# Kernel tuning notes

Hardware: AMD Instinct MI355X
Metric: run time of the kernel (lower is better)

## Reference

```python
import jax, jax.numpy as jnp
import numpy as np

WS = 8    # window size
DM = 64   # d_model
DI = 128  # d_inner = 2*d_model (expand=2)
DS = 16   # d_state
DR = 4    # dt_rank = ceil(d_model/16)
K = 4     # scan directions


def setup_inputs() -> dict:
    key = jax.random.key(0)
    ks = jax.random.split(key, 8)
    B, H, W = 2, 128, 128
    x = jax.random.normal(ks[0], (B, DM, H, W), jnp.float32)
    in_proj_w = jax.random.normal(ks[1], (2 * DI, DM), jnp.float32) * 0.02
    conv_w = jax.random.normal(ks[2], (DI, 1, 3, 3), jnp.float32) * 0.1
    conv_b = jnp.zeros((DI,), jnp.float32)
    x_proj_w = jax.random.normal(ks[3], (K, DR + 2 * DS, DI), jnp.float32) * 0.02
    dt_projs_w = jax.random.normal(ks[4], (K, DI, DR), jnp.float32) * 0.1
    dt_projs_b = jax.random.uniform(ks[5], (K, DI), jnp.float32, -6.0, -3.0)
    A_logs = jnp.log(jnp.tile(jnp.arange(1, DS + 1, dtype=jnp.float32), (K, DI, 1)))
    Ds = jnp.ones((K, DI), jnp.float32)
    ln_g = jnp.ones((DI,), jnp.float32)
    ln_b = jnp.zeros((DI,), jnp.float32)
    out_proj_w = jax.random.normal(ks[6], (DM, DI), jnp.float32) * 0.02
    return dict(x=x, in_proj_w=in_proj_w, conv_w=conv_w, conv_b=conv_b,
                x_proj_w=x_proj_w, dt_projs_w=dt_projs_w, dt_projs_b=dt_projs_b,
                A_logs=A_logs, Ds=Ds, ln_g=ln_g, ln_b=ln_b, out_proj_w=out_proj_w)


def _ss2d(x, in_proj_w, conv_w, conv_b, x_proj_w, dt_projs_w, dt_projs_b,
          A_logs, Ds, ln_g, ln_b, out_proj_w):
    # x: (Bw, DM, h, w) -- one 8x8 window per batch element
    Bw, _, h, w = x.shape
    L = h * w
    xhwc = x.transpose(0, 2, 3, 1)                      # (Bw,h,w,DM)
    xz = xhwc @ in_proj_w.T                             # (Bw,h,w,2*DI)
    xc, z = jnp.split(xz, 2, axis=-1)
    xc = xc.transpose(0, 3, 1, 2)                       # (Bw,DI,h,w)
    xc = jax.lax.conv_general_dilated(
        xc, conv_w, (1, 1), 'SAME', feature_group_count=DI,
        dimension_numbers=('NCHW', 'OIHW', 'NCHW')) + conv_b[None, :, None, None]
    xc = jax.nn.silu(xc)
    # 4-direction cross-scan: hw, wh, reversed hw, reversed wh
    x_hw = xc.reshape(Bw, DI, L)
    x_wh = xc.transpose(0, 1, 3, 2).reshape(Bw, DI, L)
    xs = jnp.stack([x_hw, x_wh, x_hw[..., ::-1], x_wh[..., ::-1]], axis=1)  # (Bw,K,DI,L)
    x_dbl = jnp.einsum('bkdl,kcd->bkcl', xs, x_proj_w)
    dt_lo, Bmat, Cmat = jnp.split(x_dbl, [DR, DR + DS], axis=2)
    dt = jnp.einsum('bkrl,kdr->bkdl', dt_lo, dt_projs_w)
    dt = jax.nn.softplus(dt + dt_projs_b[None, :, :, None])  # (Bw,K,DI,L)
    A = -jnp.exp(A_logs)                                     # (K,DI,DS)

    def step(hst, inp):
        u_t, dt_t, B_t, C_t = inp  # (Bw,K,DI),(Bw,K,DI),(Bw,K,DS),(Bw,K,DS)
        dA = jnp.exp(dt_t[..., None] * A)                       # (Bw,K,DI,DS)
        hst = hst * dA + (dt_t * u_t)[..., None] * B_t[:, :, None, :]
        y = jnp.einsum('bkds,bks->bkd', hst, C_t)
        return hst, y

    seq = (jnp.moveaxis(xs, -1, 0), jnp.moveaxis(dt, -1, 0),
           jnp.moveaxis(Bmat, -1, 0), jnp.moveaxis(Cmat, -1, 0))
    h0 = jnp.zeros((Bw, K, DI, DS), xs.dtype)
    _, ys = jax.lax.scan(step, h0, seq)                  # (L,Bw,K,DI)
    ys = jnp.moveaxis(ys, 0, -1) + Ds[None, :, :, None] * xs  # (Bw,K,DI,L)
    # merge directions (undo flips / wh transpose)
    y = (ys[:, 0]
         + ys[:, 2][..., ::-1]
         + ys[:, 1].reshape(Bw, DI, w, h).transpose(0, 1, 3, 2).reshape(Bw, DI, L)
         + ys[:, 3][..., ::-1].reshape(Bw, DI, w, h).transpose(0, 1, 3, 2).reshape(Bw, DI, L))
    y = y.reshape(Bw, DI, h, w).transpose(0, 2, 3, 1)    # (Bw,h,w,DI)
    mu = y.mean(-1, keepdims=True)
    var = y.var(-1, keepdims=True)
    y = (y - mu) * jax.lax.rsqrt(var + 1e-5) * ln_g + ln_b
    y = y * jax.nn.silu(z)
    out = y @ out_proj_w.T                               # (Bw,h,w,DM)
    return out.transpose(0, 3, 1, 2)


def reference(x, in_proj_w, conv_w, conv_b, x_proj_w, dt_projs_w, dt_projs_b,
              A_logs, Ds, ln_g, ln_b, out_proj_w):
    B, D, H, W = x.shape
    nh, nw = H // WS, W // WS
    # window partition: b d (nh hs) (nw ws) -> (b nh nw) d hs ws
    xw = x.reshape(B, D, nh, WS, nw, WS).transpose(0, 2, 4, 1, 3, 5)
    xw = xw.reshape(B * nh * nw, D, WS, WS)
    yw = _ss2d(xw, in_proj_w, conv_w, conv_b, x_proj_w, dt_projs_w, dt_projs_b,
               A_logs, Ds, ln_g, ln_b, out_proj_w)
    # window merge
    y = yw.reshape(B, nh, nw, D, WS, WS).transpose(0, 3, 1, 4, 2, 5)
    return y.reshape(B, D, H, W)
```

## Files before the change

kernel.cpp:

```cpp
#include <hip/hip_runtime.h>

#define L_HW (128*128)

__device__ __forceinline__ int transp(int p){ return ((p&7)<<3)|(p>>3); }

#define K1_XIN  0
#define K1_WBUF 4352
#define K1_XCP  8448
#define K1_XOUT 0
#define K1_SMEM 12608

__global__ __launch_bounds__(512, 4)
void k1_gemm(const float* __restrict__ x,
             const float* __restrict__ in_proj_w,
             const float* __restrict__ conv_w,
             const float* __restrict__ conv_b,
             float* __restrict__ xct_g,
             float* __restrict__ z_g)
{
    __shared__ float sm[K1_SMEM];
    const int t = threadIdx.x;
    const int win = blockIdx.x >> 2, q = blockIdx.x & 3;
    const int b = win >> 8, ih = (win >> 4) & 15, iw = win & 15;
    const float* xwin = x + ((size_t)b*64)*L_HW + ih*8*128 + iw*8;

    {
        const int ch = t >> 3, r = t & 7;
        const float* src = xwin + (size_t)ch*L_HW + r*128;
        float4 v0 = *(const float4*)(src);
        float4 v1 = *(const float4*)(src + 4);
        float* dst = sm + K1_XIN + ch;
        const int p0 = r*8;
        dst[(p0+0)*68]=v0.x; dst[(p0+1)*68]=v0.y; dst[(p0+2)*68]=v0.z; dst[(p0+3)*68]=v0.w;
        dst[(p0+4)*68]=v1.x; dst[(p0+5)*68]=v1.y; dst[(p0+6)*68]=v1.z; dst[(p0+7)*68]=v1.w;
    }
    {
        const float* wsrc = in_proj_w + q*4096;
        *(float4*)(sm + K1_WBUF + t*4)        = *(const float4*)(wsrc + t*4);
        *(float4*)(sm + K1_WBUF + (t+512)*4)  = *(const float4*)(wsrc + (t+512)*4);
    }
    __syncthreads();

    const int p = t & 63, og = t >> 6;
    float a0=0,a1=0,a2=0,a3=0,a4=0,a5=0,a6=0,a7=0;
    {
        const float* wrow = sm + K1_WBUF + og*8*64;
#define K1ACC(J, A) { float4 wv = *(const float4*)(wrow + (J)*64 + chq*4); \
        A = fmaf(xv.x,wv.x, fmaf(xv.y,wv.y, fmaf(xv.z,wv.z, fmaf(xv.w,wv.w, A)))); }
        #pragma unroll
        for (int chq = 0; chq < 16; ++chq) {
            float4 xv = *(const float4*)(sm + K1_XIN + p*68 + chq*4);
            K1ACC(0,a0) K1ACC(1,a1) K1ACC(2,a2) K1ACC(3,a3)
            K1ACC(4,a4) K1ACC(5,a5) K1ACC(6,a6) K1ACC(7,a7)
        }
#undef K1ACC
    }

    if (q >= 2) {
        float* zw = z_g + (size_t)win*8192 + ((q-2)*64)*64 + p;
        zw[(og*8+0)*64]=a0; zw[(og*8+1)*64]=a1; zw[(og*8+2)*64]=a2; zw[(og*8+3)*64]=a3;
        zw[(og*8+4)*64]=a4; zw[(og*8+5)*64]=a5; zw[(og*8+6)*64]=a6; zw[(og*8+7)*64]=a7;
        return;
    }

    {
        float* xp = sm + K1_XCP + og*8*65 + p;
        xp[0]=a0; xp[65]=a1; xp[130]=a2; xp[195]=a3;
        xp[260]=a4; xp[325]=a5; xp[390]=a6; xp[455]=a7;
    }
    __syncthreads();

    {
        const int dloc = t & 63, qq = t >> 6;
        const int dg = q*64 + dloc;
        const float* cwp = conv_w + dg*9;
        const float c0=cwp[0],c1=cwp[1],c2=cwp[2],c3=cwp[3],c4=cwp[4],
                    c5=cwp[5],c6=cwp[6],c7=cwp[7],c8=cwp[8];
        const float cb = conv_b[dg];
        const float* xc = sm + K1_XCP + dloc*65;
        #pragma unroll
        for (int jj = 0; jj < 8; ++jj) {
            const int px = qq*8 + jj;
            const int r = px >> 3, c = px & 7;
            float a = cb;
            if (r > 0) {
                if (c > 0) a = fmaf(xc[px-9], c0, a);
                a = fmaf(xc[px-8], c1, a);
                if (c < 7) a = fmaf(xc[px-7], c2, a);
            }
            if (c > 0) a = fmaf(xc[px-1], c3, a);
            a = fmaf(xc[px], c4, a);
            if (c < 7) a = fmaf(xc[px+1], c5, a);
            if (r < 7) {
                if (c > 0) a = fmaf(xc[px+7], c6, a);
                a = fmaf(xc[px+8], c7, a);
                if (c < 7) a = fmaf(xc[px+9], c8, a);
            }
            sm[K1_XOUT + px*68 + dloc] = a / (1.f + __expf(-a));
        }
    }
    __syncthreads();

    {
        float* dst = xct_g + (size_t)win*8192 + q*64;
        #pragma unroll
        for (int i = 0; i < 2; ++i) {
            const int idx4 = i*512 + t;
            const int pp = idx4 >> 4, dg = idx4 & 15;
            float4 v = *(const float4*)(sm + K1_XOUT + pp*68 + dg*4);
            *(float4*)(dst + pp*128 + dg*4) = v;
        }
    }
}

#define K2_WL 4096
#define K2_XD 6400
#define K2_SMEM 8768

__global__ __launch_bounds__(256, 4)
void k2_xproj(const float* __restrict__ xct_g,
              const float* __restrict__ x_proj_w,
              float* __restrict__ xdbl_g)
{
    __shared__ float sm[K2_SMEM];
    const int t = threadIdx.x;
    const int win = blockIdx.x >> 2, k = blockIdx.x & 3;
    const int p = t & 63, jg = t >> 6;
    float a0=0,a1=0,a2=0,a3=0,a4=0,a5=0,a6=0,a7=0,a8=0;

    for (int h = 0; h < 2; ++h) {
        __syncthreads();
        #pragma unroll
        for (int i = 0; i < 4; ++i) {
            const int idx4 = i*256 + t;
            const int pp = idx4 >> 4, dg = idx4 & 15;
            float4 v = *(const float4*)(xct_g + (size_t)win*8192 + pp*128 + h*64 + dg*4);
            *(float4*)(sm + pp*64 + ((dg ^ (pp&7))<<2)) = v;
        }
        #pragma unroll
        for (int i = 0; i < 3; ++i) {
            const int idx4 = i*256 + t;
            if (idx4 < 576) {
                const int r = idx4 >> 4, dg = idx4 & 15;
                float4 v = *(const float4*)(x_proj_w + (size_t)(k*36 + r)*128 + h*64 + dg*4);
                *(float4*)(sm + K2_WL + r*64 + dg*4) = v;
            }
        }
        __syncthreads();
        const float* wb = sm + K2_WL + jg*9*64;
#define K2ACC(J, A) { float4 wv = *(const float4*)(wb + (J)*64 + dg*4); \
        A = fmaf(xv.x,wv.x, fmaf(xv.y,wv.y, fmaf(xv.z,wv.z, fmaf(xv.w,wv.w, A)))); }
        #pragma unroll
        for (int dg = 0; dg < 16; ++dg) {
            float4 xv = *(const float4*)(sm + p*64 + ((dg ^ (p&7))<<2));
            K2ACC(0,a0) K2ACC(1,a1) K2ACC(2,a2) K2ACC(3,a3) K2ACC(4,a4)
            K2ACC(5,a5) K2ACC(6,a6) K2ACC(7,a7) K2ACC(8,a8)
        }
#undef K2ACC
    }
    __syncthreads();

    {
        const int l = (k==0) ? p : (k==1) ? transp(p) : (k==2) ? (63-p) : (63 - transp(p));
        float* dp = sm + K2_XD + l*37 + jg*9;
        dp[0]=a0; dp[1]=a1; dp[2]=a2; dp[3]=a3; dp[4]=a4;
        dp[5]=a5; dp[6]=a6; dp[7]=a7; dp[8]=a8;
    }
    __syncthreads();

    {
        float* dst = xdbl_g + ((size_t)win*4 + k)*2304;
        #pragma unroll
        for (int i = 0; i < 9; ++i) {
            const int idx = i*256 + t;
            const int l2 = idx / 36, c = idx - l2*36;
            dst[idx] = sm[K2_XD + l2*37 + c];
        }
    }
}

#define F_XD 0
#define F_YM 0
#define F_U  9216
#define F_MU 17408
#define F_RS 17472
#define F_SMEM 17536

#define HSTEP(I, E, BC, CC) { h##I = fmaf(h##I, (E), dtu*(BC)); y = fmaf(h##I, (CC), y); }

__global__ __launch_bounds__(512, 4)
void k3_all(const float* __restrict__ xct_g,
            const float* __restrict__ z_g,
            const float* __restrict__ xdbl_g,
            const float* __restrict__ dt_projs_w,
            const float* __restrict__ dt_projs_b,
            const float* __restrict__ A_logs,
            const float* __restrict__ Ds,
            const float* __restrict__ ln_g,
            const float* __restrict__ ln_b,
            const float* __restrict__ out_proj_w,
            float* __restrict__ y_g,
            float* __restrict__ out)
{
    __shared__ float sm[F_SMEM];
    const int t = threadIdx.x;
    const int win = blockIdx.x;

    #pragma unroll
    for (int i = 0; i < 5; ++i) {
        const int idx4 = i*512 + t;
        if (idx4 < 2304) {
            float4 v = *(const float4*)(xdbl_g + (size_t)win*9216 + idx4*4);
            *(float4*)(sm + F_XD + idx4*4) = v;
        }
    }
    #pragma unroll
    for (int i = 0; i < 4; ++i) {
        const int idx4 = i*512 + t;
        float4 v = *(const float4*)(xct_g + (size_t)win*8192 + idx4*4);
        *(float4*)(sm + F_U + idx4*4) = v;
    }
    __syncthreads();

    {
        const int k = t >> 7, d = t & 127;
        const int kd = t;
        const float* alp = A_logs + kd*16;
        const float A0 = -__expf(alp[0]);
        bool fast = true;
        #pragma unroll
        for (int s = 1; s < 16; ++s) {
            float a = -__expf(alp[s]);
            fast = fast && (fabsf(a - (float)(s+1)*A0) <= 1e-4f * fabsf(a));
        }
        const float4 wv = *(const float4*)(dt_projs_w + kd*4);
        const float dtb = dt_projs_b[kd];
        float h0=0,h1=0,h2=0,h3=0,h4=0,h5=0,h6=0,h7=0,
              h8=0,h9=0,h10=0,h11=0,h12=0,h13=0,h14=0,h15=0;
        const float* XDk = sm + F_XD + k*2304;
        const float* ul = sm + F_U + d;
        float* yw = y_g + ((size_t)win*4 + k)*8192 + d;

        if (fast) {
            for (int l = 0; l < 64; ++l) {
                const float* row = XDk + l*36;
                float4 d4 = *(const float4*)(row);
                float4 b0 = *(const float4*)(row+4),  b1 = *(const float4*)(row+8);
                float4 b2 = *(const float4*)(row+12), b3 = *(const float4*)(row+16);
                float4 c0 = *(const float4*)(row+20), c1 = *(const float4*)(row+24);
                float4 c2 = *(const float4*)(row+28), c3 = *(const float4*)(row+32);
                float dtraw = dtb + wv.x*d4.x + wv.y*d4.y + wv.z*d4.z + wv.w*d4.w;
                float dt = (dtraw > 20.f) ? dtraw : __logf(1.f + __expf(dtraw));
                const int lr = 63 - l;
                const int p = (k==0)?l : (k==1)?transp(l) : (k==2)?lr : transp(lr);
                const float u = ul[p*128];
                const float dtu = dt * u;
                const float r  = __expf(dt * A0);
                const float r2 = r*r, r4 = r2*r2, r8 = r4*r4;
                const float e3 = r2*r, e5 = r4*r, e6 = r4*r2, e7 = r4*e3;
                const float e9 = r8*r, e10 = r8*r2, e11 = r8*e3, e12 = r8*r4;
                const float e13 = r8*e5, e14 = r8*e6, e15 = r8*e7, e16 = r8*r8;
                float y = 0.f;
                HSTEP(0,  r,   b0.x, c0.x)  HSTEP(1,  r2,  b0.y, c0.y)
                HSTEP(2,  e3,  b0.z, c0.z)  HSTEP(3,  r4,  b0.w, c0.w)
                HSTEP(4,  e5,  b1.x, c1.x)  HSTEP(5,  e6,  b1.y, c1.y)
                HSTEP(6,  e7,  b1.z, c1.z)  HSTEP(7,  r8,  b1.w, c1.w)
                HSTEP(8,  e9,  b2.x, c2.x)  HSTEP(9,  e10, b2.y, c2.y)
                HSTEP(10, e11, b2.z, c2.z)  HSTEP(11, e12, b2.w, c2.w)
                HSTEP(12, e13, b3.x, c3.x)  HSTEP(13, e14, b3.y, c3.y)
                HSTEP(14, e15, b3.z, c3.z)  HSTEP(15, e16, b3.w, c3.w)
                yw[l*128] = y;
            }
        } else {
            const float A1=-__expf(alp[1]), A2=-__expf(alp[2]), A3=-__expf(alp[3]),
                        A4=-__expf(alp[4]), A5=-__expf(alp[5]), A6=-__expf(alp[6]),
                        A7=-__expf(alp[7]), A8=-__expf(alp[8]), A9=-__expf(alp[9]),
                        A10=-__expf(alp[10]), A11=-__expf(alp[11]), A12=-__expf(alp[12]),
                        A13=-__expf(alp[13]), A14=-__expf(alp[14]), A15=-__expf(alp[15]);
            for (int l = 0; l < 64; ++l) {
                const float* row = XDk + l*36;
                float4 d4 = *(const float4*)(row);
                float4 b0 = *(const float4*)(row+4),  b1 = *(const float4*)(row+8);
                float4 b2 = *(const float4*)(row+12), b3 = *(const float4*)(row+16);
                float4 c0 = *(const float4*)(row+20), c1 = *(const float4*)(row+24);
                float4 c2 = *(const float4*)(row+28), c3 = *(const float4*)(row+32);
                float dtraw = dtb + wv.x*d4.x + wv.y*d4.y + wv.z*d4.z + wv.w*d4.w;
                float dt = (dtraw > 20.f) ? dtraw : __logf(1.f + __expf(dtraw));
                const int lr = 63 - l;
                const int p = (k==0)?l : (k==1)?transp(l) : (k==2)?lr : transp(lr);
                const float u = ul[p*128];
                const float dtu = dt * u;
                float y = 0.f;
                HSTEP(0,  __expf(dt*A0),  b0.x, c0.x)  HSTEP(1,  __expf(dt*A1),  b0.y, c0.y)
                HSTEP(2,  __expf(dt*A2),  b0.z, c0.z)  HSTEP(3,  __expf(dt*A3),  b0.w, c0.w)
                HSTEP(4,  __expf(dt*A4),  b1.x, c1.x)  HSTEP(5,  __expf(dt*A5),  b1.y, c1.y)
                HSTEP(6,  __expf(dt*A6),  b1.z, c1.z)  HSTEP(7,  __expf(dt*A7),  b1.w, c1.w)
                HSTEP(8,  __expf(dt*A8),  b2.x, c2.x)  HSTEP(9,  __expf(dt*A9),  b2.y, c2.y)
                HSTEP(10, __expf(dt*A10), b2.z, c2.z)  HSTEP(11, __expf(dt*A11), b2.w, c2.w)
                HSTEP(12, __expf(dt*A12), b3.x, c3.x)  HSTEP(13, __expf(dt*A13), b3.y, c3.y)
                HSTEP(14, __expf(dt*A14), b3.z, c3.z)  HSTEP(15, __expf(dt*A15), b3.w, c3.w)
                yw[l*128] = y;
            }
        }
    }
    __syncthreads();

    {
        const int d2 = t & 127, pq = t >> 7;
        const float Dsum = Ds[d2] + Ds[128+d2] + Ds[256+d2] + Ds[384+d2];
        const float* yg0 = y_g + ((size_t)win*4 + 0)*8192 + d2;
        const float* yg1 = y_g + ((size_t)win*4 + 1)*8192 + d2;
        const float* yg2 = y_g + ((size_t)win*4 + 2)*8192 + d2;
        const float* yg3 = y_g + ((size_t)win*4 + 3)*8192 + d2;
        const float* uc  = sm + F_U + d2;
        #pragma unroll
        for (int i = 0; i < 16; ++i) {
            const int p = pq*16 + i;
            const int tp = transp(p);
            float v = yg0[p*128] + yg1[tp*128] + yg2[(63-p)*128] + yg3[(63-tp)*128]
                    + Dsum * uc[p*128];
            sm[F_YM + d2*65 + p] = v;
        }
    }
    __syncthreads();

    {
        const int px = t >> 3, j = t & 7;
        float s1 = 0.f, s2 = 0.f;
        #pragma unroll
        for (int i = 0; i < 16; ++i) {
            float v = sm[F_YM + (j*16 + i)*65 + px];
            s1 += v; s2 += v*v;
        }
        s1 += __shfl_xor(s1,1); s2 += __shfl_xor(s2,1);
        s1 += __shfl_xor(s1,2); s2 += __shfl_xor(s2,2);
        s1 += __shfl_xor(s1,4); s2 += __shfl_xor(s2,4);
        if (j == 0) {
            float mu  = s1 * 0.0078125f;
            float var = s2 * 0.0078125f - mu*mu;
            sm[F_MU + px] = mu;
            sm[F_RS + px] = rsqrtf(var + 1e-5f);
        }
    }
    __syncthreads();

    {
        const int p = t & 63, dblk = (t >> 6) * 16;
        const float mu = sm[F_MU + p], rs = sm[F_RS + p];
        const float* zb = z_g + (size_t)win*8192 + p;
        #pragma unroll
        for (int i = 0; i < 16; ++i) {
            const int d = dblk + i;
            float yv = sm[F_YM + d*65 + p];
            float yh = (yv - mu)*rs*ln_g[d] + ln_b[d];
            float zv = zb[d*64];
            sm[F_YM + d*65 + p] = yh * (zv / (1.f + __expf(-zv)));
        }
    }
    __syncthreads();

    {
        const int p = t & 63, m0 = (t >> 6) * 8;
        float o0=0,o1=0,o2=0,o3=0,o4=0,o5=0,o6=0,o7=0;
#define OACC(J, O) { float4 wq = *(const float4*)(out_proj_w + (m0+(J))*128 + dq*4); \
        O = fmaf(y0,wq.x, fmaf(y1,wq.y, fmaf(y2,wq.z, fmaf(y3,wq.w, O)))); }
        #pragma unroll
        for (int dq = 0; dq < 32; ++dq) {
            float y0 = sm[F_YM + (dq*4+0)*65 + p];
            float y1 = sm[F_YM + (dq*4+1)*65 + p];
            float y2 = sm[F_YM + (dq*4+2)*65 + p];
            float y3 = sm[F_YM + (dq*4+3)*65 + p];
            OACC(0,o0) OACC(1,o1) OACC(2,o2) OACC(3,o3)
            OACC(4,o4) OACC(5,o5) OACC(6,o6) OACC(7,o7)
        }
#undef OACC
        const int b = win >> 8, ih = (win>>4)&15, iw = win&15;
        float* op = out + ((size_t)b*64)*L_HW + (ih*8 + (p>>3))*128 + iw*8 + (p&7);
        op[(size_t)(m0+0)*L_HW]=o0; op[(size_t)(m0+1)*L_HW]=o1;
        op[(size_t)(m0+2)*L_HW]=o2; op[(size_t)(m0+3)*L_HW]=o3;
        op[(size_t)(m0+4)*L_HW]=o4; op[(size_t)(m0+5)*L_HW]=o5;
        op[(size_t)(m0+6)*L_HW]=o6; op[(size_t)(m0+7)*L_HW]=o7;
    }
}
#undef HSTEP

extern "C" void kernel_launch(void* const* d_in, const int* in_sizes, int n_in,
                              void* d_out, int out_size, void* d_ws, size_t ws_size,
                              hipStream_t stream) {
    const float* x          = (const float*)d_in[0];
    const float* in_proj_w  = (const float*)d_in[1];
    const float* conv_w     = (const float*)d_in[2];
    const float* conv_b     = (const float*)d_in[3];
    const float* x_proj_w   = (const float*)d_in[4];
    const float* dt_projs_w = (const float*)d_in[5];
    const float* dt_projs_b = (const float*)d_in[6];
    const float* A_logs     = (const float*)d_in[7];
    const float* Ds         = (const float*)d_in[8];
    const float* ln_g       = (const float*)d_in[9];
    const float* ln_b       = (const float*)d_in[10];
    const float* out_proj_w = (const float*)d_in[11];
    float* out = (float*)d_out;

    float* xct  = (float*)d_ws;
    float* zb   = xct + 4194304;
    float* xdbl = zb  + 4194304;
    float* yg   = xdbl + 1179648;

    k1_gemm<<<dim3(2048), dim3(512), 0, stream>>>(x, in_proj_w, conv_w, conv_b, xct, zb);
    k2_xproj<<<dim3(2048), dim3(256), 0, stream>>>(xct, x_proj_w, xdbl);
    k3_all<<<dim3(512), dim3(512), 0, stream>>>(
        xct, zb, xdbl, dt_projs_w, dt_projs_b, A_logs, Ds, ln_g, ln_b,
        out_proj_w, yg, out);
}
```

Measured before the change: 157.3 us.

## Merge scan directions in shared memory instead of round-tripping through global

The selective scan no longer writes per-direction outputs to a global y buffer and reads them back. Each thread writes its step output to a small shared staging area every 4 steps, and 128 threads then accumulate the four directions into the merged shared tile. The u input is read straight from global instead of being staged in shared memory, and the per-step y sum is split into four accumulators to shorten the dependency chain. The cost is two block barriers per 4-step chunk (32 in total) and a serial merge by a quarter of the threads.

```diff
diff --git a/kernel.cpp b/kernel.cpp
--- a/kernel.cpp
+++ b/kernel.cpp
@@ -180,13 +180,13 @@
 }
 
 #define F_XD 0
-#define F_YM 0
-#define F_U  9216
-#define F_MU 17408
-#define F_RS 17472
-#define F_SMEM 17536
-
-#define HSTEP(I, E, BC, CC) { h##I = fmaf(h##I, (E), dtu*(BC)); y = fmaf(h##I, (CC), y); }
+#define F_YC 9216
+#define F_YM 11264
+#define F_MU 19584
+#define F_RS 19648
+#define F_SMEM 19712
+
+#define HSTEP(I, E, BC, CC, Y) { h##I = fmaf(h##I, (E), dtu*(BC)); Y = fmaf(h##I, (CC), Y); }
 
 __global__ __launch_bounds__(512, 4)
 void k3_all(const float* __restrict__ xct_g,
@@ -199,7 +199,6 @@
             const float* __restrict__ ln_g,
             const float* __restrict__ ln_b,
             const float* __restrict__ out_proj_w,
-            float* __restrict__ y_g,
             float* __restrict__ out)
 {
     __shared__ float sm[F_SMEM];
@@ -214,38 +213,53 @@
             *(float4*)(sm + F_XD + idx4*4) = v;
         }
     }
+    for (int i = t; i < 8320; i += 512) sm[F_YM + i] = 0.f;
+
+    const int k = t >> 7, d = t & 127;
+    const int kd = t;
+    const float* alp = A_logs + kd*16;
+    const float A0 = -__expf(alp[0]);
+    bool fastp = true;
     #pragma unroll
-    for (int i = 0; i < 4; ++i) {
-        const int idx4 = i*512 + t;
-        float4 v = *(const float4*)(xct_g + (size_t)win*8192 + idx4*4);
-        *(float4*)(sm + F_U + idx4*4) = v;
-    }
-    __syncthreads();
-
-    {
-        const int k = t >> 7, d = t & 127;
-        const int kd = t;
-        const float* alp = A_logs + kd*16;
-        const float A0 = -__expf(alp[0]);
-        bool fast = true;
-        #pragma unroll
-        for (int s = 1; s < 16; ++s) {
-            float a = -__expf(alp[s]);
-            fast = fast && (fabsf(a - (float)(s+1)*A0) <= 1e-4f * fabsf(a));
-        }
-        const float4 wv = *(const float4*)(dt_projs_w + kd*4);
-        const float dtb = dt_projs_b[kd];
-        float h0=0,h1=0,h2=0,h3=0,h4=0,h5=0,h6=0,h7=0,
-              h8=0,h9=0,h10=0,h11=0,h12=0,h13=0,h14=0,h15=0;
-        const float* XDk = sm + F_XD + k*2304;
-        const float* ul = sm + F_U + d;
-        float* yw = y_g + ((size_t)win*4 + k)*8192 + d;
-
-        if (fast) {
-            for (int l = 0; l < 64; ++l) {
+    for (int s = 1; s < 16; ++s) {
+        float a = -__expf(alp[s]);
+        fastp = fastp && (fabsf(a - (float)(s+1)*A0) <= 1e-4f * fabsf(a));
+    }
+    const int allfast = __syncthreads_and(fastp ? 1 : 0);
+
+    const float4 wv = *(const float4*)(dt_projs_w + kd*4);
+    const float dtb = dt_projs_b[kd];
+    float h0=0,h1=0,h2=0,h3=0,h4=0,h5=0,h6=0,h7=0,
+          h8=0,h9=0,h10=0,h11=0,h12=0,h13=0,h14=0,h15=0;
+    const float* XDk = sm + F_XD + k*2304;
+    const float* ub = xct_g + (size_t)win*8192 + d;
+
+#define MERGE_CHUNK(C) { \
+        __syncthreads(); \
+        if (t < 128) { \
+            const int dd = t; \
+            float* ymr = sm + F_YM + dd*65; \
+            _Pragma("unroll") \
+            for (int j = 0; j < 4; ++j) { \
+                const int l = (C)*4 + j; \
+                const int lr = 63 - l; \
+                const float* ycb = sm + F_YC + j*512 + dd; \
+                ymr[l]          += ycb[0]; \
+                ymr[transp(l)]  += ycb[128]; \
+                ymr[lr]         += ycb[256]; \
+                ymr[transp(lr)] += ycb[384]; \
+            } \
+        } \
+        __syncthreads(); }
+
+    if (allfast) {
+        for (int c = 0; c < 16; ++c) {
+            #pragma unroll
+            for (int j = 0; j < 4; ++j) {
+                const int l = c*4 + j;
                 const float* row = XDk + l*36;
                 float4 d4 = *(const float4*)(row);
-                float4 b0 = *(const float4*)(row+4),  b1 = *(const float4*)(row+8);
+                float4 b0 = *(const float4*)(row+4),  float4_b1 = *(const float4*)(row+8);
                 float4 b2 = *(const float4*)(row+12), b3 = *(const float4*)(row+16);
                 float4 c0 = *(const float4*)(row+20), c1 = *(const float4*)(row+24);
                 float4 c2 = *(const float4*)(row+28), c3 = *(const float4*)(row+32);
@@ -253,34 +267,39 @@
                 float dt = (dtraw > 20.f) ? dtraw : __logf(1.f + __expf(dtraw));
                 const int lr = 63 - l;
                 const int p = (k==0)?l : (k==1)?transp(l) : (k==2)?lr : transp(lr);
-                const float u = ul[p*128];
+                const float u = ub[p*128];
                 const float dtu = dt * u;
                 const float r  = __expf(dt * A0);
                 const float r2 = r*r, r4 = r2*r2, r8 = r4*r4;
                 const float e3 = r2*r, e5 = r4*r, e6 = r4*r2, e7 = r4*e3;
                 const float e9 = r8*r, e10 = r8*r2, e11 = r8*e3, e12 = r8*r4;
                 const float e13 = r8*e5, e14 = r8*e6, e15 = r8*e7, e16 = r8*r8;
-                float y = 0.f;
-                HSTEP(0,  r,   b0.x, c0.x)  HSTEP(1,  r2,  b0.y, c0.y)
-                HSTEP(2,  e3,  b0.z, c0.z)  HSTEP(3,  r4,  b0.w, c0.w)
-                HSTEP(4,  e5,  b1.x, c1.x)  HSTEP(5,  e6,  b1.y, c1.y)
-                HSTEP(6,  e7,  b1.z, c1.z)  HSTEP(7,  r8,  b1.w, c1.w)
-                HSTEP(8,  e9,  b2.x, c2.x)  HSTEP(9,  e10, b2.y, c2.y)
-                HSTEP(10, e11, b2.z, c2.z)  HSTEP(11, e12, b2.w, c2.w)
-                HSTEP(12, e13, b3.x, c3.x)  HSTEP(13, e14, b3.y, c3.y)
-                HSTEP(14, e15, b3.z, c3.z)  HSTEP(15, e16, b3.w, c3.w)
-                yw[l*128] = y;
+                float ay0 = 0.f, ay1 = 0.f, ay2 = 0.f, ay3 = 0.f;
+                HSTEP(0,  r,   b0.x, c0.x, ay0)  HSTEP(1,  r2,  b0.y, c0.y, ay1)
+                HSTEP(2,  e3,  b0.z, c0.z, ay2)  HSTEP(3,  r4,  b0.w, c0.w, ay3)
+                HSTEP(4,  e5,  float4_b1.x, c1.x, ay0)  HSTEP(5,  e6,  float4_b1.y, c1.y, ay1)
+                HSTEP(6,  e7,  float4_b1.z, c1.z, ay2)  HSTEP(7,  r8,  float4_b1.w, c1.w, ay3)
+                HSTEP(8,  e9,  b2.x, c2.x, ay0)  HSTEP(9,  e10, b2.y, c2.y, ay1)
+                HSTEP(10, e11, b2.z, c2.z, ay2)  HSTEP(11, e12, b2.w, c2.w, ay3)
+                HSTEP(12, e13, b3.x, c3.x, ay0)  HSTEP(13, e14, b3.y, c3.y, ay1)
+                HSTEP(14, e15, b3.z, c3.z, ay2)  HSTEP(15, e16, b3.w, c3.w, ay3)
+                sm[F_YC + j*512 + t] = (ay0 + ay1) + (ay2 + ay3);
             }
-        } else {
-            const float A1=-__expf(alp[1]), A2=-__expf(alp[2]), A3=-__expf(alp[3]),
-                        A4=-__expf(alp[4]), A5=-__expf(alp[5]), A6=-__expf(alp[6]),
-                        A7=-__expf(alp[7]), A8=-__expf(alp[8]), A9=-__expf(alp[9]),
-                        A10=-__expf(alp[10]), A11=-__expf(alp[11]), A12=-__expf(alp[12]),
-                        A13=-__expf(alp[13]), A14=-__expf(alp[14]), A15=-__expf(alp[15]);
-            for (int l = 0; l < 64; ++l) {
+            MERGE_CHUNK(c)
+        }
+    } else {
+        const float A1=-__expf(alp[1]), A2=-__expf(alp[2]), A3=-__expf(alp[3]),
+                    A4=-__expf(alp[4]), A5=-__expf(alp[5]), A6=-__expf(alp[6]),
+                    A7=-__expf(alp[7]), A8=-__expf(alp[8]), A9=-__expf(alp[9]),
+                    A10=-__expf(alp[10]), A11=-__expf(alp[11]), A12=-__expf(alp[12]),
+                    A13=-__expf(alp[13]), A14=-__expf(alp[14]), A15=-__expf(alp[15]);
+        for (int c = 0; c < 16; ++c) {
+            #pragma unroll
+            for (int j = 0; j < 4; ++j) {
+                const int l = c*4 + j;
                 const float* row = XDk + l*36;
                 float4 d4 = *(const float4*)(row);
-                float4 b0 = *(const float4*)(row+4),  b1 = *(const float4*)(row+8);
+                float4 b0 = *(const float4*)(row+4),  float4_b1 = *(const float4*)(row+8);
                 float4 b2 = *(const float4*)(row+12), b3 = *(const float4*)(row+16);
                 float4 c0 = *(const float4*)(row+20), c1 = *(const float4*)(row+24);
                 float4 c2 = *(const float4*)(row+28), c3 = *(const float4*)(row+32);
@@ -288,38 +307,32 @@
                 float dt = (dtraw > 20.f) ? dtraw : __logf(1.f + __expf(dtraw));
                 const int lr = 63 - l;
                 const int p = (k==0)?l : (k==1)?transp(l) : (k==2)?lr : transp(lr);
-                const float u = ul[p*128];
+                const float u = ub[p*128];
                 const float dtu = dt * u;
-                float y = 0.f;
-                HSTEP(0,  __expf(dt*A0),  b0.x, c0.x)  HSTEP(1,  __expf(dt*A1),  b0.y, c0.y)
-                HSTEP(2,  __expf(dt*A2),  b0.z, c0.z)  HSTEP(3,  __expf(dt*A3),  b0.w, c0.w)
-                HSTEP(4,  __expf(dt*A4),  b1.x, c1.x)  HSTEP(5,  __expf(dt*A5),  b1.y, c1.y)
-                HSTEP(6,  __expf(dt*A6),  b1.z, c1.z)  HSTEP(7,  __expf(dt*A7),  b1.w, c1.w)
-                HSTEP(8,  __expf(dt*A8),  b2.x, c2.x)  HSTEP(9,  __expf(dt*A9),  b2.y, c2.y)
-                HSTEP(10, __expf(dt*A10), b2.z, c2.z)  HSTEP(11, __expf(dt*A11), b2.w, c2.w)
-                HSTEP(12, __expf(dt*A12), b3.x, c3.x)  HSTEP(13, __expf(dt*A13), b3.y, c3.y)
-                HSTEP(14, __expf(dt*A14), b3.z, c3.z)  HSTEP(15, __expf(dt*A15), b3.w, c3.w)
-                yw[l*128] = y;
+                float ay0 = 0.f, ay1 = 0.f, ay2 = 0.f, ay3 = 0.f;
+                HSTEP(0,  __expf(dt*A0),  b0.x, c0.x, ay0)  HSTEP(1,  __expf(dt*A1),  b0.y, c0.y, ay1)
+                HSTEP(2,  __expf(dt*A2),  b0.z, c0.z, ay2)  HSTEP(3,  __expf(dt*A3),  b0.w, c0.w, ay3)
+                HSTEP(4,  __expf(dt*A4),  float4_b1.x, c1.x, ay0)  HSTEP(5,  __expf(dt*A5),  float4_b1.y, c1.y, ay1)
+                HSTEP(6,  __expf(dt*A6),  float4_b1.z, c1.z, ay2)  HSTEP(7,  __expf(dt*A7),  float4_b1.w, c1.w, ay3)
+                HSTEP(8,  __expf(dt*A8),  b2.x, c2.x, ay0)  HSTEP(9,  __expf(dt*A9),  b2.y, c2.y, ay1)
+                HSTEP(10, __expf(dt*A10), b2.z, c2.z, ay2)  HSTEP(11, __expf(dt*A11), b2.w, c2.w, ay3)
+                HSTEP(12, __expf(dt*A12), b3.x, c3.x, ay0)  HSTEP(13, __expf(dt*A13), b3.y, c3.y, ay1)
+                HSTEP(14, __expf(dt*A14), b3.z, c3.z, ay2)  HSTEP(15, __expf(dt*A15), b3.w, c3.w, ay3)
+                sm[F_YC + j*512 + t] = (ay0 + ay1) + (ay2 + ay3);
             }
-        }
-    }
-    __syncthreads();
+            MERGE_CHUNK(c)
+        }
+    }
+#undef MERGE_CHUNK
 
     {
         const int d2 = t & 127, pq = t >> 7;
         const float Dsum = Ds[d2] + Ds[128+d2] + Ds[256+d2] + Ds[384+d2];
-        const float* yg0 = y_g + ((size_t)win*4 + 0)*8192 + d2;
-        const float* yg1 = y_g + ((size_t)win*4 + 1)*8192 + d2;
-        const float* yg2 = y_g + ((size_t)win*4 + 2)*8192 + d2;
-        const float* yg3 = y_g + ((size_t)win*4 + 3)*8192 + d2;
-        const float* uc  = sm + F_U + d2;
+        const float* uc = xct_g + (size_t)win*8192 + d2;
         #pragma unroll
         for (int i = 0; i < 16; ++i) {
             const int p = pq*16 + i;
-            const int tp = transp(p);
-            float v = yg0[p*128] + yg1[tp*128] + yg2[(63-p)*128] + yg3[(63-tp)*128]
-                    + Dsum * uc[p*128];
-            sm[F_YM + d2*65 + p] = v;
+            sm[F_YM + d2*65 + p] += Dsum * uc[p*128];
         }
     }
     __syncthreads();
@@ -350,11 +363,11 @@
         const float* zb = z_g + (size_t)win*8192 + p;
         #pragma unroll
         for (int i = 0; i < 16; ++i) {
-            const int d = dblk + i;
-            float yv = sm[F_YM + d*65 + p];
-            float yh = (yv - mu)*rs*ln_g[d] + ln_b[d];
-            float zv = zb[d*64];
-            sm[F_YM + d*65 + p] = yh * (zv / (1.f + __expf(-zv)));
+            const int dd = dblk + i;
+            float yv = sm[F_YM + dd*65 + p];
+            float yh = (yv - mu)*rs*ln_g[dd] + ln_b[dd];
+            float zv = zb[dd*64];
+            sm[F_YM + dd*65 + p] = yh * (zv / (1.f + __expf(-zv)));
         }
     }
     __syncthreads();
@@ -404,11 +417,10 @@
     float* xct  = (float*)d_ws;
     float* zb   = xct + 4194304;
     float* xdbl = zb  + 4194304;
-    float* yg   = xdbl + 1179648;
 
     k1_gemm<<<dim3(2048), dim3(512), 0, stream>>>(x, in_proj_w, conv_w, conv_b, xct, zb);
     k2_xproj<<<dim3(2048), dim3(256), 0, stream>>>(xct, x_proj_w, xdbl);
     k3_all<<<dim3(512), dim3(512), 0, stream>>>(
         xct, zb, xdbl, dt_projs_w, dt_projs_b, A_logs, Ds, ln_g, ln_b,
-        out_proj_w, yg, out);
+        out_proj_w, out);
 }
```

New measurement: 164.1 us. 1.04x slower.

## Store scan outputs in spatial order and merge directions with vectorized loads

Applied to the files above, without the earlier changes.

The selective-scan stage now writes each direction's output at its un-permuted spatial position. The merge step can then read the four direction buffers with contiguous float4 loads instead of scattered transposed/reversed gathers. The fast-path choice is made block-uniform with __syncthreads_and, and the per-position y accumulation is split into four independent chains to shorten the FMA dependency. The Ds sum is precomputed once into shared memory. This adds a small shared buffer, and the global scan writes are now scattered per direction.

```diff
diff --git a/kernel.cpp b/kernel.cpp
--- a/kernel.cpp
+++ b/kernel.cpp
@@ -184,9 +184,10 @@
 #define F_U  9216
 #define F_MU 17408
 #define F_RS 17472
-#define F_SMEM 17536
-
-#define HSTEP(I, E, BC, CC) { h##I = fmaf(h##I, (E), dtu*(BC)); y = fmaf(h##I, (CC), y); }
+#define F_DS 17536
+#define F_SMEM 17664
+
+#define HSTEP(I, E, BC, CC, Y) { h##I = fmaf(h##I, (E), dtu*(BC)); Y = fmaf(h##I, (CC), Y); }
 
 __global__ __launch_bounds__(512, 4)
 void k3_all(const float* __restrict__ xct_g,
@@ -220,106 +221,108 @@
         float4 v = *(const float4*)(xct_g + (size_t)win*8192 + idx4*4);
         *(float4*)(sm + F_U + idx4*4) = v;
     }
-    __syncthreads();
-
-    {
-        const int k = t >> 7, d = t & 127;
-        const int kd = t;
-        const float* alp = A_logs + kd*16;
-        const float A0 = -__expf(alp[0]);
-        bool fast = true;
-        #pragma unroll
-        for (int s = 1; s < 16; ++s) {
-            float a = -__expf(alp[s]);
-            fast = fast && (fabsf(a - (float)(s+1)*A0) <= 1e-4f * fabsf(a));
-        }
-        const float4 wv = *(const float4*)(dt_projs_w + kd*4);
-        const float dtb = dt_projs_b[kd];
-        float h0=0,h1=0,h2=0,h3=0,h4=0,h5=0,h6=0,h7=0,
-              h8=0,h9=0,h10=0,h11=0,h12=0,h13=0,h14=0,h15=0;
-        const float* XDk = sm + F_XD + k*2304;
-        const float* ul = sm + F_U + d;
-        float* yw = y_g + ((size_t)win*4 + k)*8192 + d;
-
-        if (fast) {
-            for (int l = 0; l < 64; ++l) {
-                const float* row = XDk + l*36;
-                float4 d4 = *(const float4*)(row);
-                float4 b0 = *(const float4*)(row+4),  b1 = *(const float4*)(row+8);
-                float4 b2 = *(const float4*)(row+12), b3 = *(const float4*)(row+16);
-                float4 c0 = *(const float4*)(row+20), c1 = *(const float4*)(row+24);
-                float4 c2 = *(const float4*)(row+28), c3 = *(const float4*)(row+32);
-                float dtraw = dtb + wv.x*d4.x + wv.y*d4.y + wv.z*d4.z + wv.w*d4.w;
-                float dt = (dtraw > 20.f) ? dtraw : __logf(1.f + __expf(dtraw));
-                const int lr = 63 - l;
-                const int p = (k==0)?l : (k==1)?transp(l) : (k==2)?lr : transp(lr);
-                const float u = ul[p*128];
-                const float dtu = dt * u;
-                const float r  = __expf(dt * A0);
-                const float r2 = r*r, r4 = r2*r2, r8 = r4*r4;
-                const float e3 = r2*r, e5 = r4*r, e6 = r4*r2, e7 = r4*e3;
-                const float e9 = r8*r, e10 = r8*r2, e11 = r8*e3, e12 = r8*r4;
-                const float e13 = r8*e5, e14 = r8*e6, e15 = r8*e7, e16 = r8*r8;
-                float y = 0.f;
-                HSTEP(0,  r,   b0.x, c0.x)  HSTEP(1,  r2,  b0.y, c0.y)
-                HSTEP(2,  e3,  b0.z, c0.z)  HSTEP(3,  r4,  b0.w, c0.w)
-                HSTEP(4,  e5,  b1.x, c1.x)  HSTEP(5,  e6,  b1.y, c1.y)
-                HSTEP(6,  e7,  b1.z, c1.z)  HSTEP(7,  r8,  b1.w, c1.w)
-                HSTEP(8,  e9,  b2.x, c2.x)  HSTEP(9,  e10, b2.y, c2.y)
-                HSTEP(10, e11, b2.z, c2.z)  HSTEP(11, e12, b2.w, c2.w)
-                HSTEP(12, e13, b3.x, c3.x)  HSTEP(13, e14, b3.y, c3.y)
-                HSTEP(14, e15, b3.z, c3.z)  HSTEP(15, e16, b3.w, c3.w)
-                yw[l*128] = y;
-            }
-        } else {
-            const float A1=-__expf(alp[1]), A2=-__expf(alp[2]), A3=-__expf(alp[3]),
-                        A4=-__expf(alp[4]), A5=-__expf(alp[5]), A6=-__expf(alp[6]),
-                        A7=-__expf(alp[7]), A8=-__expf(alp[8]), A9=-__expf(alp[9]),
-                        A10=-__expf(alp[10]), A11=-__expf(alp[11]), A12=-__expf(alp[12]),
-                        A13=-__expf(alp[13]), A14=-__expf(alp[14]), A15=-__expf(alp[15]);
-            for (int l = 0; l < 64; ++l) {
-                const float* row = XDk + l*36;
-                float4 d4 = *(const float4*)(row);
-                float4 b0 = *(const float4*)(row+4),  b1 = *(const float4*)(row+8);
-                float4 b2 = *(const float4*)(row+12), b3 = *(const float4*)(row+16);
-                float4 c0 = *(const float4*)(row+20), c1 = *(const float4*)(row+24);
-                float4 c2 = *(const float4*)(row+28), c3 = *(const float4*)(row+32);
-                float dtraw = dtb + wv.x*d4.x + wv.y*d4.y + wv.z*d4.z + wv.w*d4.w;
-                float dt = (dtraw > 20.f) ? dtraw : __logf(1.f + __expf(dtraw));
-                const int lr = 63 - l;
-                const int p = (k==0)?l : (k==1)?transp(l) : (k==2)?lr : transp(lr);
-                const float u = ul[p*128];
-                const float dtu = dt * u;
-                float y = 0.f;
-                HSTEP(0,  __expf(dt*A0),  b0.x, c0.x)  HSTEP(1,  __expf(dt*A1),  b0.y, c0.y)
-                HSTEP(2,  __expf(dt*A2),  b0.z, c0.z)  HSTEP(3,  __expf(dt*A3),  b0.w, c0.w)
-                HSTEP(4,  __expf(dt*A4),  b1.x, c1.x)  HSTEP(5,  __expf(dt*A5),  b1.y, c1.y)
-                HSTEP(6,  __expf(dt*A6),  b1.z, c1.z)  HSTEP(7,  __expf(dt*A7),  b1.w, c1.w)
-                HSTEP(8,  __expf(dt*A8),  b2.x, c2.x)  HSTEP(9,  __expf(dt*A9),  b2.y, c2.y)
-                HSTEP(10, __expf(dt*A10), b2.z, c2.z)  HSTEP(11, __expf(dt*A11), b2.w, c2.w)
-                HSTEP(12, __expf(dt*A12), b3.x, c3.x)  HSTEP(13, __expf(dt*A13), b3.y, c3.y)
-                HSTEP(14, __expf(dt*A14), b3.z, c3.z)  HSTEP(15, __expf(dt*A15), b3.w, c3.w)
-                yw[l*128] = y;
-            }
-        }
-    }
-    __syncthreads();
-
-    {
-        const int d2 = t & 127, pq = t >> 7;
-        const float Dsum = Ds[d2] + Ds[128+d2] + Ds[256+d2] + Ds[384+d2];
-        const float* yg0 = y_g + ((size_t)win*4 + 0)*8192 + d2;
-        const float* yg1 = y_g + ((size_t)win*4 + 1)*8192 + d2;
-        const float* yg2 = y_g + ((size_t)win*4 + 2)*8192 + d2;
-        const float* yg3 = y_g + ((size_t)win*4 + 3)*8192 + d2;
-        const float* uc  = sm + F_U + d2;
-        #pragma unroll
-        for (int i = 0; i < 16; ++i) {
-            const int p = pq*16 + i;
-            const int tp = transp(p);
-            float v = yg0[p*128] + yg1[tp*128] + yg2[(63-p)*128] + yg3[(63-tp)*128]
-                    + Dsum * uc[p*128];
-            sm[F_YM + d2*65 + p] = v;
+    if (t < 128) sm[F_DS + t] = Ds[t] + Ds[128+t] + Ds[256+t] + Ds[384+t];
+
+    const int k = t >> 7, d = t & 127;
+    const int kd = t;
+    const float* alp = A_logs + kd*16;
+    const float A0 = -__expf(alp[0]);
+    bool fastp = true;
+    #pragma unroll
+    for (int s = 1; s < 16; ++s) {
+        float a = -__expf(alp[s]);
+        fastp = fastp && (fabsf(a - (float)(s+1)*A0) <= 1e-4f * fabsf(a));
+    }
+    const int allfast = __syncthreads_and(fastp ? 1 : 0);
+
+    const float4 wv = *(const float4*)(dt_projs_w + kd*4);
+    const float dtb = dt_projs_b[kd];
+    float h0=0,h1=0,h2=0,h3=0,h4=0,h5=0,h6=0,h7=0,
+          h8=0,h9=0,h10=0,h11=0,h12=0,h13=0,h14=0,h15=0;
+    const float* XDk = sm + F_XD + k*2304;
+    const float* ul = sm + F_U + d;
+    float* yw = y_g + ((size_t)win*4 + k)*8192 + d;
+
+    if (allfast) {
+        for (int l = 0; l < 64; ++l) {
+            const float* row = XDk + l*36;
+            float4 d4 = *(const float4*)(row);
+            float4 b0 = *(const float4*)(row+4),  b1 = *(const float4*)(row+8);
+            float4 b2 = *(const float4*)(row+12), b3 = *(const float4*)(row+16);
+            float4 c0 = *(const float4*)(row+20), c1 = *(const float4*)(row+24);
+            float4 c2 = *(const float4*)(row+28), c3 = *(const float4*)(row+32);
+            float dtraw = dtb + wv.x*d4.x + wv.y*d4.y + wv.z*d4.z + wv.w*d4.w;
+            float dt = (dtraw > 20.f) ? dtraw : __logf(1.f + __expf(dtraw));
+            const int lr = 63 - l;
+            const int p = (k==0)?l : (k==1)?transp(l) : (k==2)?lr : transp(lr);
+            const float u = ul[p*128];
+            const float dtu = dt * u;
+            const float r  = __expf(dt * A0);
+            const float r2 = r*r, r4 = r2*r2, r8 = r4*r4;
+            const float e3 = r2*r, e5 = r4*r, e6 = r4*r2, e7 = r4*e3;
+            const float e9 = r8*r, e10 = r8*r2, e11 = r8*e3, e12 = r8*r4;
+            const float e13 = r8*e5, e14 = r8*e6, e15 = r8*e7, e16 = r8*r8;
+            float ay0=0.f, ay1=0.f, ay2=0.f, ay3=0.f;
+            HSTEP(0,  r,   b0.x, c0.x, ay0)  HSTEP(1,  r2,  b0.y, c0.y, ay1)
+            HSTEP(2,  e3,  b0.z, c0.z, ay2)  HSTEP(3,  r4,  b0.w, c0.w, ay3)
+            HSTEP(4,  e5,  b1.x, c1.x, ay0)  HSTEP(5,  e6,  b1.y, c1.y, ay1)
+            HSTEP(6,  e7,  b1.z, c1.z, ay2)  HSTEP(7,  r8,  b1.w, c1.w, ay3)
+            HSTEP(8,  e9,  b2.x, c2.x, ay0)  HSTEP(9,  e10, b2.y, c2.y, ay1)
+            HSTEP(10, e11, b2.z, c2.z, ay2)  HSTEP(11, e12, b2.w, c2.w, ay3)
+            HSTEP(12, e13, b3.x, c3.x, ay0)  HSTEP(13, e14, b3.y, c3.y, ay1)
+            HSTEP(14, e15, b3.z, c3.z, ay2)  HSTEP(15, e16, b3.w, c3.w, ay3)
+            yw[p*128] = (ay0 + ay1) + (ay2 + ay3);
+        }
+    } else {
+        const float A1=-__expf(alp[1]), A2=-__expf(alp[2]), A3=-__expf(alp[3]),
+                    A4=-__expf(alp[4]), A5=-__expf(alp[5]), A6=-__expf(alp[6]),
+                    A7=-__expf(alp[7]), A8=-__expf(alp[8]), A9=-__expf(alp[9]),
+                    A10=-__expf(alp[10]), A11=-__expf(alp[11]), A12=-__expf(alp[12]),
+                    A13=-__expf(alp[13]), A14=-__expf(alp[14]), A15=-__expf(alp[15]);
+        for (int l = 0; l < 64; ++l) {
+            const float* row = XDk + l*36;
+            float4 d4 = *(const float4*)(row);
+            float4 b0 = *(const float4*)(row+4),  b1 = *(const float4*)(row+8);
+            float4 b2 = *(const float4*)(row+12), b3 = *(const float4*)(row+16);
+            float4 c0 = *(const float4*)(row+20), c1 = *(const float4*)(row+24);
+            float4 c2 = *(const float4*)(row+28), c3 = *(const float4*)(row+32);
+            float dtraw = dtb + wv.x*d4.x + wv.y*d4.y + wv.z*d4.z + wv.w*d4.w;
+            float dt = (dtraw > 20.f) ? dtraw : __logf(1.f + __expf(dtraw));
+            const int lr = 63 - l;
+            const int p = (k==0)?l : (k==1)?transp(l) : (k==2)?lr : transp(lr);
+            const float u = ul[p*128];
+            const float dtu = dt * u;
+            float ay0=0.f, ay1=0.f, ay2=0.f, ay3=0.f;
+            HSTEP(0,  __expf(dt*A0),  b0.x, c0.x, ay0)  HSTEP(1,  __expf(dt*A1),  b0.y, c0.y, ay1)
+            HSTEP(2,  __expf(dt*A2),  b0.z, c0.z, ay2)  HSTEP(3,  __expf(dt*A3),  b0.w, c0.w, ay3)
+            HSTEP(4,  __expf(dt*A4),  b1.x, c1.x, ay0)  HSTEP(5,  __expf(dt*A5),  b1.y, c1.y, ay1)
+            HSTEP(6,  __expf(dt*A6),  b1.z, c1.z, ay2)  HSTEP(7,  __expf(dt*A7),  b1.w, c1.w, ay3)
+            HSTEP(8,  __expf(dt*A8),  b2.x, c2.x, ay0)  HSTEP(9,  __expf(dt*A9),  b2.y, c2.y, ay1)
+            HSTEP(10, __expf(dt*A10), b2.z, c2.z, ay2)  HSTEP(11, __expf(dt*A11), b2.w, c2.w, ay3)
+            HSTEP(12, __expf(dt*A12), b3.x, c3.x, ay0)  HSTEP(13, __expf(dt*A13), b3.y, c3.y, ay1)
+            HSTEP(14, __expf(dt*A14), b3.z, c3.z, ay2)  HSTEP(15, __expf(dt*A15), b3.w, c3.w, ay3)
+            yw[p*128] = (ay0 + ay1) + (ay2 + ay3);
+        }
+    }
+    __syncthreads();
+
+    {
+        const float* yb = y_g + (size_t)win*32768;
+        #pragma unroll
+        for (int i = 0; i < 4; ++i) {
+            const int idx = i*512 + t;
+            const int p = idx >> 5, dq = idx & 31;
+            float4 v0 = *(const float4*)(yb +           p*128 + dq*4);
+            float4 v1 = *(const float4*)(yb +  8192  +  p*128 + dq*4);
+            float4 v2 = *(const float4*)(yb +  16384 +  p*128 + dq*4);
+            float4 v3 = *(const float4*)(yb +  24576 +  p*128 + dq*4);
+            float4 u4 = *(const float4*)(sm + F_U + p*128 + dq*4);
+            float4 ds4 = *(const float4*)(sm + F_DS + dq*4);
+            float* ymc = sm + F_YM + (dq*4)*65 + p;
+            ymc[0]   = v0.x+v1.x+v2.x+v3.x + ds4.x*u4.x;
+            ymc[65]  = v0.y+v1.y+v2.y+v3.y + ds4.y*u4.y;
+            ymc[130] = v0.z+v1.z+v2.z+v3.z + ds4.z*u4.z;
+            ymc[195] = v0.w+v1.w+v2.w+v3.w + ds4.w*u4.w;
         }
     }
     __syncthreads();
@@ -350,11 +353,11 @@
         const float* zb = z_g + (size_t)win*8192 + p;
         #pragma unroll
         for (int i = 0; i < 16; ++i) {
-            const int d = dblk + i;
-            float yv = sm[F_YM + d*65 + p];
-            float yh = (yv - mu)*rs*ln_g[d] + ln_b[d];
-            float zv = zb[d*64];
-            sm[F_YM + d*65 + p] = yh * (zv / (1.f + __expf(-zv)));
+            const int dd = dblk + i;
+            float yv = sm[F_YM + dd*65 + p];
+            float yh = (yv - mu)*rs*ln_g[dd] + ln_b[dd];
+            float zv = zb[dd*64];
+            sm[F_YM + dd*65 + p] = yh * (zv / (1.f + __expf(-zv)));
         }
     }
     __syncthreads();
```

New measurement: 169.1 us. 7.5% more time.
